# Optimization experiments

Hardware: AMD Instinct MI355X
Metric: run time of the kernel (lower is better)

Reference implementation:

```python
import jax, jax.numpy as jnp
import numpy as np

N_NODES, N_FEAT, HIDDEN, N_EDGES, N_GRAPHS = 50000, 128, 64, 800000, 64
BN_EPS = 1e-5


def setup_inputs() -> dict:
    key = jax.random.key(0)
    ks = jax.random.split(key, 12)
    x = jax.random.normal(ks[0], (N_NODES, N_FEAT), jnp.float32)
    edge_index = jax.random.randint(ks[1], (2, N_EDGES), 0, N_NODES, jnp.int32)
    batch = jnp.sort(jax.random.randint(ks[2], (N_NODES,), 0, N_GRAPHS, jnp.int32))
    s_in = 1.0 / np.sqrt(N_FEAT)
    s_h = 1.0 / np.sqrt(HIDDEN)
    return {
        "x": x,
        "edge_index": edge_index,
        "batch": batch,
        "W_in": jax.random.normal(ks[3], (HIDDEN, N_FEAT), jnp.float32) * s_in,
        "W1": jax.random.normal(ks[4], (HIDDEN, N_FEAT), jnp.float32) * s_in,
        "b1": jnp.zeros((HIDDEN,), jnp.float32),
        "Ws": jax.random.normal(ks[5], (4, HIDDEN, HIDDEN), jnp.float32) * s_h,
        "bs": jnp.zeros((4, HIDDEN), jnp.float32),
        "bn_gamma": jnp.ones((5, HIDDEN), jnp.float32),
        "bn_beta": jnp.zeros((5, HIDDEN), jnp.float32),
        "bn_mean": jnp.zeros((5, HIDDEN), jnp.float32),
        "bn_var": jnp.ones((5, HIDDEN), jnp.float32),
        "lin_w": jax.random.normal(ks[6], (1, HIDDEN), jnp.float32) * s_h,
        "lin_b": jnp.zeros((1,), jnp.float32),
    }


def reference(x, edge_index, batch, W_in, W1, b1, Ws, bs, bn_gamma, bn_beta, bn_mean, bn_var, lin_w, lin_b):
    N = x.shape[0]
    # add self loops (GCNConv default), symmetric normalization D^-1/2 (A+I) D^-1/2
    loop = jnp.arange(N, dtype=edge_index.dtype)
    src = jnp.concatenate([edge_index[0], loop])  # [E+N]
    dst = jnp.concatenate([edge_index[1], loop])
    deg = jax.ops.segment_sum(jnp.ones_like(dst, jnp.float32), dst, num_segments=N)
    dinv = jax.lax.rsqrt(deg)  # deg >= 1 due to self-loops
    norm = dinv[src] * dinv[dst]  # [E+N]

    def gcn(h, W, b):
        h = h @ W.T                          # [N, H]
        msg = h[src] * norm[:, None]          # gather + edge scaling
        out = jax.ops.segment_sum(msg, dst, num_segments=N)  # scatter-add
        return out + b

    def bn(h, i):
        # eval-mode BatchNorm1d with running stats
        return (h - bn_mean[i]) * (bn_gamma[i] * jax.lax.rsqrt(bn_var[i] + BN_EPS)) + bn_beta[i]

    identity = x @ W_in.T  # input projection for residual
    # layer 1 (dropout = identity in eval)
    h = jax.nn.relu(bn(gcn(x, W1, b1), 0)) + identity
    # layers 2-4 with residual
    for i in range(3):
        h = jax.nn.relu(bn(gcn(h, Ws[i], bs[i]), i + 1)) + h
    # layer 5, no residual afterwards
    h = jax.nn.relu(bn(gcn(h, Ws[3], bs[3]), 4))

    # global mean pool over graphs
    sums = jax.ops.segment_sum(h, batch, num_segments=N_GRAPHS)
    cnts = jax.ops.segment_sum(jnp.ones((N,), jnp.float32), batch, num_segments=N_GRAPHS)
    pooled = sums / jnp.maximum(cnts, 1.0)[:, None]  # [G, H]
    return pooled @ lin_w.T + lin_b  # [G, 1]
```

## Files before the change

### kernel.cpp

```cpp
#include <hip/hip_runtime.h>
#include <hip/hip_fp16.h>

#define N_NODES 50000
#define N_FEAT  128
#define HID     64
#define N_EDGES 800000
#define N_GRAPHS 64
#define MAXDEG  64
#define BN_EPS  1e-5f
#define NB256(n) (((n) + 255) / 256)

__global__ __launch_bounds__(256) void k_zero(int* fill) {
    int i = blockIdx.x * 256 + threadIdx.x;
    if (i < N_NODES) fill[i] = 0;
}

#define GE_NB 2500
__global__ __launch_bounds__(256) void k_gemmedge(const int* __restrict__ ei,
                                                  int* fill, unsigned short* __restrict__ colp,
                                                  const float* __restrict__ x,
                                                  const float* __restrict__ W_in,
                                                  const float* __restrict__ W1,
                                                  float* __restrict__ h,
                                                  __half* __restrict__ g16) {
    __shared__ float4 Wt[2][8 * 65];
    __shared__ float4 xs[20 * 32];
    const int bid = blockIdx.x;
    const int t = threadIdx.x;

    const int ebase = bid * 320;
    int s1 = ei[ebase + t];
    int d1 = ei[N_EDGES + ebase + t];
    int k1 = atomicAdd(&fill[d1], 1);
    int s2 = 0, d2 = 0, k2 = MAXDEG;
    if (t < 64) {
        s2 = ei[ebase + 256 + t];
        d2 = ei[N_EDGES + ebase + 256 + t];
        k2 = atomicAdd(&fill[d2], 1);
    }

    const float4* W0v = (const float4*)W_in;
    const float4* W1v = (const float4*)W1;
    const int h2a = t >> 3, k4a = t & 7;
    const int h2b = h2a + 32;
    float4 w0a = W0v[h2a * 32 + k4a];
    float4 w1a = W1v[h2a * 32 + k4a];
    float4 w0b = W0v[h2b * 32 + k4a];
    float4 w1b = W1v[h2b * 32 + k4a];

    const int base = bid * 20;
    const float4* xv = (const float4*)(x + (long long)base * N_FEAT);
    for (int i = t; i < 20 * 32; i += 256) xs[i] = xv[i];

    const int hh = t & 63;
    const int ng = t >> 6;
    float4 a0[5], a1[5];
#pragma unroll
    for (int j = 0; j < 5; ++j) {
        a0[j] = make_float4(0.f, 0.f, 0.f, 0.f);
        a1[j] = make_float4(0.f, 0.f, 0.f, 0.f);
    }

    for (int c = 0; c < 32; c += 8) {
        __syncthreads();
        Wt[0][k4a * 65 + h2a] = w0a;  Wt[1][k4a * 65 + h2a] = w1a;
        Wt[0][k4a * 65 + h2b] = w0b;  Wt[1][k4a * 65 + h2b] = w1b;
        if (c + 8 < 32) {
            w0a = W0v[h2a * 32 + c + 8 + k4a]; w1a = W1v[h2a * 32 + c + 8 + k4a];
            w0b = W0v[h2b * 32 + c + 8 + k4a]; w1b = W1v[h2b * 32 + c + 8 + k4a];
        }
        __syncthreads();
#pragma unroll
        for (int k4 = 0; k4 < 8; ++k4) {
            float4 w0 = Wt[0][k4 * 65 + hh];
            float4 w1 = Wt[1][k4 * 65 + hh];
#pragma unroll
            for (int j = 0; j < 5; ++j) {
                float4 xx = xs[(ng + 4 * j) * 32 + c + k4];
                a0[j].x += w0.x * xx.x; a0[j].y += w0.y * xx.y;
                a0[j].z += w0.z * xx.z; a0[j].w += w0.w * xx.w;
                a1[j].x += w1.x * xx.x; a1[j].y += w1.y * xx.y;
                a1[j].z += w1.z * xx.z; a1[j].w += w1.w * xx.w;
            }
        }
    }
#pragma unroll
    for (int j = 0; j < 5; ++j) {
        int node = base + ng + 4 * j;
        h[node * HID + hh]   = a0[j].x + a0[j].y + a0[j].z + a0[j].w;
        g16[node * HID + hh] = __float2half(a1[j].x + a1[j].y + a1[j].z + a1[j].w);
    }

    if (k1 < MAXDEG) colp[d1 * MAXDEG + k1] = (unsigned short)s1;
    if (k2 < MAXDEG) colp[d2 * MAXDEG + k2] = (unsigned short)s2;
}

__device__ __forceinline__ void acc8s(const uint4 r, float* a, float s) {
    float2 f0 = __half22float2(*(const __half2*)&r.x);
    float2 f1 = __half22float2(*(const __half2*)&r.y);
    float2 f2 = __half22float2(*(const __half2*)&r.z);
    float2 f3 = __half22float2(*(const __half2*)&r.w);
    a[0] += s * f0.x; a[1] += s * f0.y; a[2] += s * f1.x; a[3] += s * f1.y;
    a[4] += s * f2.x; a[5] += s * f2.y; a[6] += s * f3.x; a[7] += s * f3.y;
}

template <bool NSCALE, bool DOGEMM>
__global__ __launch_bounds__(256, 4) void k_gather_fused(const __half* __restrict__ gin,
                                                      const unsigned short* __restrict__ colp,
                                                      const int* __restrict__ fill,
                                                      const float* __restrict__ b,
                                                      const float* __restrict__ gamma,
                                                      const float* __restrict__ beta,
                                                      const float* __restrict__ mean,
                                                      const float* __restrict__ var,
                                                      const float4* __restrict__ res4,
                                                      float4* __restrict__ h4,
                                                      const float* __restrict__ W,
                                                      __half* __restrict__ gout) {
    __shared__ float4 Wt[DOGEMM ? 16 * 65 : 1];
    __shared__ float4 hrow[DOGEMM ? 32 * 17 : 1];

    const int t = threadIdx.x;
    const int wv = t >> 6;
    const int lane = t & 63;
    const int hh8 = lane & 7;
    const int sub = lane >> 3;
    const int nl = wv * 8 + sub;
    const int n = blockIdx.x * 32 + nl;
    const bool nvalid = (n < N_NODES);

    if (DOGEMM) {
        const float4* Wv = (const float4*)W;
        for (int i = t; i < HID * 16; i += 256) {
            int h2 = i >> 4, k4 = i & 15;
            Wt[k4 * 65 + h2] = Wv[i];
        }
        __syncthreads();
    }

    const uint4* gv = (const uint4*)gin;
    const int fl = nvalid ? fill[n] : 0;
    const int deg = fl < MAXDEG ? fl : MAXDEG;

    float a[8];
#pragma unroll
    for (int i = 0; i < 8; ++i) a[i] = 0.f;

    const uint4* cp8 = (const uint4*)(colp + (size_t)n * MAXDEG);

#pragma unroll 1
    for (int rb = 0; rb < MAXDEG; rb += 8) {
        if (!__any(rb < deg)) break;
        if (rb < deg) {
            uint4 cc = cp8[rb >> 3];
            unsigned cw[4] = {cc.x, cc.y, cc.z, cc.w};
            int c[8]; float s[8]; uint4 v[8];
#pragma unroll
            for (int k = 0; k < 8; ++k) {
                bool pk = (rb + k) < deg;
                int col = (int)((cw[k >> 1] >> (16 * (k & 1))) & 0xFFFFu);
                c[k] = pk ? col : 0;
                if (NSCALE) s[k] = pk ? rsqrtf((float)fill[c[k]] + 1.0f) : 0.0f;
                else        s[k] = pk ? 1.0f : 0.0f;
            }
#pragma unroll
            for (int k = 0; k < 8; ++k) v[k] = gv[(size_t)c[k] * 8 + hh8];
#pragma unroll
            for (int k = 0; k < 8; ++k) acc8s(v[k], a, s[k]);
        }
    }

    const float di = rsqrtf((float)fl + 1.0f);
    if (nvalid) acc8s(gv[(size_t)n * 8 + hh8], a, NSCALE ? di : 1.0f);

    float o[8];
    {
        float4 b0 = ((const float4*)b)[hh8 * 2],     b1 = ((const float4*)b)[hh8 * 2 + 1];
        float4 g0 = ((const float4*)gamma)[hh8 * 2], g1 = ((const float4*)gamma)[hh8 * 2 + 1];
        float4 e0 = ((const float4*)beta)[hh8 * 2],  e1 = ((const float4*)beta)[hh8 * 2 + 1];
        float4 m0 = ((const float4*)mean)[hh8 * 2],  m1 = ((const float4*)mean)[hh8 * 2 + 1];
        float4 v0 = ((const float4*)var)[hh8 * 2],   v1 = ((const float4*)var)[hh8 * 2 + 1];
        float bb[8] = {b0.x, b0.y, b0.z, b0.w, b1.x, b1.y, b1.z, b1.w};
        float gg[8] = {g0.x, g0.y, g0.z, g0.w, g1.x, g1.y, g1.z, g1.w};
        float ee[8] = {e0.x, e0.y, e0.z, e0.w, e1.x, e1.y, e1.z, e1.w};
        float mm[8] = {m0.x, m0.y, m0.z, m0.w, m1.x, m1.y, m1.z, m1.w};
        float vv[8] = {v0.x, v0.y, v0.z, v0.w, v1.x, v1.y, v1.z, v1.w};
#pragma unroll
        for (int i = 0; i < 8; ++i) {
            float sc = gg[i] * rsqrtf(vv[i] + BN_EPS);
            float sh = (bb[i] - mm[i]) * sc + ee[i];
            o[i] = fmaxf(fmaf(a[i] * di, sc, sh), 0.f);
        }
    }

    if (res4 != nullptr && nvalid) {
        float4 r0 = res4[(size_t)n * 16 + hh8 * 2];
        float4 r1 = res4[(size_t)n * 16 + hh8 * 2 + 1];
        o[0] += r0.x; o[1] += r0.y; o[2] += r0.z; o[3] += r0.w;
        o[4] += r1.x; o[5] += r1.y; o[6] += r1.z; o[7] += r1.w;
    }

    float4 lo = make_float4(o[0], o[1], o[2], o[3]);
    float4 hi = make_float4(o[4], o[5], o[6], o[7]);
    if (nvalid) {
        h4[(size_t)n * 16 + hh8 * 2]     = lo;
        h4[(size_t)n * 16 + hh8 * 2 + 1] = hi;
    }

    if (DOGEMM) {
        hrow[nl * 17 + hh8 * 2]     = lo;
        hrow[nl * 17 + hh8 * 2 + 1] = hi;
        const int hh = lane;
        const int nb = blockIdx.x * 32 + wv * 8;
        float acc[8];
#pragma unroll
        for (int s8 = 0; s8 < 8; ++s8) acc[s8] = 0.f;
#pragma unroll 2
        for (int k4 = 0; k4 < 16; ++k4) {
            float4 w = Wt[k4 * 65 + hh];
#pragma unroll
            for (int s8 = 0; s8 < 8; ++s8) {
                float4 hv = hrow[(wv * 8 + s8) * 17 + k4];
                acc[s8] += hv.x * w.x + hv.y * w.y + hv.z * w.z + hv.w * w.w;
            }
        }
#pragma unroll
        for (int s8 = 0; s8 < 8; ++s8) {
            int ns = nb + s8;
            if (ns < N_NODES) {
                float dd = rsqrtf((float)fill[ns] + 1.0f);
                gout[(size_t)ns * HID + hh] = __float2half(acc[s8] * dd);
            }
        }
    }
}

__device__ __forceinline__ int lowerb(const int* __restrict__ b, int val) {
    int lo = 0, hi = N_NODES;
    while (lo < hi) {
        int mid = (lo + hi) >> 1;
        if (b[mid] < val) lo = mid + 1; else hi = mid;
    }
    return lo;
}

__global__ __launch_bounds__(1024) void k_poolfinal(const float* __restrict__ h,
                                                    const int* __restrict__ batch,
                                                    const float* __restrict__ lin_w,
                                                    const float* __restrict__ lin_b,
                                                    float* __restrict__ out) {
    __shared__ float red[16][HID];
    int g = blockIdx.x;
    int w = threadIdx.x >> 6;
    int hh = threadIdx.x & 63;
    int start = lowerb(batch, g);
    int end = lowerb(batch, g + 1);
    int len = end - start;
    float acc = 0.f;
    for (int n = start + w; n < end; n += 16) acc += h[n * HID + hh];
    red[w][hh] = acc;
    __syncthreads();
    if (w == 0) {
        float s = 0.f;
#pragma unroll
        for (int i = 0; i < 16; ++i) s += red[i][hh];
        float c = fmaxf((float)len, 1.0f);
        float v = (s / c) * lin_w[hh];
#pragma unroll
        for (int off = 32; off > 0; off >>= 1) v += __shfl_down(v, off);
        if (hh == 0) out[g] = v + lin_b[0];
    }
}

extern "C" void kernel_launch(void* const* d_in, const int* in_sizes, int n_in,
                              void* d_out, int out_size, void* d_ws, size_t ws_size,
                              hipStream_t stream) {
    const float* x     = (const float*)d_in[0];
    const int*   ei    = (const int*)d_in[1];
    const int*   batch = (const int*)d_in[2];
    const float* W_in  = (const float*)d_in[3];
    const float* W1    = (const float*)d_in[4];
    const float* b1    = (const float*)d_in[5];
    const float* Ws    = (const float*)d_in[6];
    const float* bs_   = (const float*)d_in[7];
    const float* bn_g  = (const float*)d_in[8];
    const float* bn_b  = (const float*)d_in[9];
    const float* bn_m  = (const float*)d_in[10];
    const float* bn_v  = (const float*)d_in[11];
    const float* lin_w = (const float*)d_in[12];
    const float* lin_b = (const float*)d_in[13];
    float* out = (float*)d_out;

    char* q = (char*)d_ws;
    int*            fill = (int*)q;             q += (size_t)50048 * 4;
    unsigned short* colp = (unsigned short*)q;  q += (size_t)N_NODES * MAXDEG * 2;
    __half*         g16a = (__half*)q;          q += (size_t)N_NODES * HID * 2;
    __half*         g16b = (__half*)q;          q += (size_t)N_NODES * HID * 2;
    float*          h    = (float*)q;           q += (size_t)N_NODES * HID * 4;

    const int NB_N  = NB256(N_NODES);
    const int NB_GA = (N_NODES + 31) / 32;
    float4* h4 = (float4*)h;

    k_zero<<<NB_N, 256, 0, stream>>>(fill);
    k_gemmedge<<<GE_NB, 256, 0, stream>>>(ei, fill, colp, x, W_in, W1, h, g16a);

    k_gather_fused<true, true><<<NB_GA, 256, 0, stream>>>(
        g16a, colp, fill, b1, bn_g, bn_b, bn_m, bn_v,
        (const float4*)h, h4, Ws + 0 * HID * HID, g16b);

    k_gather_fused<false, true><<<NB_GA, 256, 0, stream>>>(
        g16b, colp, fill, bs_ + 0 * HID,
        bn_g + 1 * HID, bn_b + 1 * HID, bn_m + 1 * HID, bn_v + 1 * HID,
        (const float4*)h, h4, Ws + 1 * HID * HID, g16a);

    k_gather_fused<false, true><<<NB_GA, 256, 0, stream>>>(
        g16a, colp, fill, bs_ + 1 * HID,
        bn_g + 2 * HID, bn_b + 2 * HID, bn_m + 2 * HID, bn_v + 2 * HID,
        (const float4*)h, h4, Ws + 2 * HID * HID, g16b);

    k_gather_fused<false, true><<<NB_GA, 256, 0, stream>>>(
        g16b, colp, fill, bs_ + 2 * HID,
        bn_g + 3 * HID, bn_b + 3 * HID, bn_m + 3 * HID, bn_v + 3 * HID,
        (const float4*)h, h4, Ws + 3 * HID * HID, g16a);

    k_gather_fused<false, false><<<NB_GA, 256, 0, stream>>>(
        g16a, colp, fill, bs_ + 3 * HID,
        bn_g + 4 * HID, bn_b + 4 * HID, bn_m + 4 * HID, bn_v + 4 * HID,
        nullptr, h4, nullptr, nullptr);

    k_poolfinal<<<N_GRAPHS, 1024, 0, stream>>>(h, batch, lin_w, lin_b, out);
}
```

Baseline: 311.0 us.

## Assign one wavefront per node with edge-parallel gather and shuffle reduction

Restructures the fused gather kernel so that each 64-lane wavefront handles one node rather than eight. The eight lane groups each process a different edge and are combined with xor-shuffle reductions. The column indices are loaded once per wave and distributed by shuffle, and the next edge's fetch is software-pipelined ahead of the accumulation. The aim is to balance load across nodes of varying degree and raise memory-level parallelism. The cost is 8x more blocks and a full W transpose into shared memory for every 4 nodes, which adds LDS traffic and per-block overhead. Bounds checks are removed, which relies on N_NODES being divisible by 4.

```diff
diff --git a/kernel.cpp b/kernel.cpp
--- a/kernel.cpp
+++ b/kernel.cpp
@@ -105,7 +105,7 @@
 }
 
 template <bool NSCALE, bool DOGEMM>
-__global__ __launch_bounds__(256, 4) void k_gather_fused(const __half* __restrict__ gin,
+__global__ __launch_bounds__(256) void k_gather_fused(const __half* __restrict__ gin,
                                                       const unsigned short* __restrict__ colp,
                                                       const int* __restrict__ fill,
                                                       const float* __restrict__ b,
@@ -118,16 +118,14 @@
                                                       const float* __restrict__ W,
                                                       __half* __restrict__ gout) {
     __shared__ float4 Wt[DOGEMM ? 16 * 65 : 1];
-    __shared__ float4 hrow[DOGEMM ? 32 * 17 : 1];
+    __shared__ float4 hrow[DOGEMM ? 4 * 17 : 1];
 
     const int t = threadIdx.x;
     const int wv = t >> 6;
     const int lane = t & 63;
+    const int egrp = lane >> 3;
     const int hh8 = lane & 7;
-    const int sub = lane >> 3;
-    const int nl = wv * 8 + sub;
-    const int n = blockIdx.x * 32 + nl;
-    const bool nvalid = (n < N_NODES);
+    const int n = blockIdx.x * 4 + wv;
 
     if (DOGEMM) {
         const float4* Wv = (const float4*)W;
@@ -135,43 +133,52 @@
             int h2 = i >> 4, k4 = i & 15;
             Wt[k4 * 65 + h2] = Wv[i];
         }
-        __syncthreads();
     }
 
     const uint4* gv = (const uint4*)gin;
-    const int fl = nvalid ? fill[n] : 0;
+    const int fl = fill[n];
     const int deg = fl < MAXDEG ? fl : MAXDEG;
 
+    int colall = (int)colp[(size_t)n * MAXDEG + lane];
+    const uint4 vself = gv[(size_t)n * 8 + hh8];
+
     float a[8];
 #pragma unroll
     for (int i = 0; i < 8; ++i) a[i] = 0.f;
 
-    const uint4* cp8 = (const uint4*)(colp + (size_t)n * MAXDEG);
-
+    const int nit = (deg + 7) >> 3;
+
+#define FETCH_E(IT, C, S, V)                                              \
+    {                                                                     \
+        int j = ((IT) << 3) + egrp;                                       \
+        int cc = __shfl(colall, j & 63);                                  \
+        bool pv = j < deg;                                                \
+        C = pv ? cc : 0;                                                  \
+        if (NSCALE) S = pv ? rsqrtf((float)fill[C] + 1.0f) : 0.0f;        \
+        else        S = pv ? 1.0f : 0.0f;                                 \
+        V = gv[(size_t)C * 8 + hh8];                                      \
+    }
+
+    int cA; float sA; uint4 vA;
+    FETCH_E(0, cA, sA, vA);
 #pragma unroll 1
-    for (int rb = 0; rb < MAXDEG; rb += 8) {
-        if (!__any(rb < deg)) break;
-        if (rb < deg) {
-            uint4 cc = cp8[rb >> 3];
-            unsigned cw[4] = {cc.x, cc.y, cc.z, cc.w};
-            int c[8]; float s[8]; uint4 v[8];
-#pragma unroll
-            for (int k = 0; k < 8; ++k) {
-                bool pk = (rb + k) < deg;
-                int col = (int)((cw[k >> 1] >> (16 * (k & 1))) & 0xFFFFu);
-                c[k] = pk ? col : 0;
-                if (NSCALE) s[k] = pk ? rsqrtf((float)fill[c[k]] + 1.0f) : 0.0f;
-                else        s[k] = pk ? 1.0f : 0.0f;
-            }
-#pragma unroll
-            for (int k = 0; k < 8; ++k) v[k] = gv[(size_t)c[k] * 8 + hh8];
-#pragma unroll
-            for (int k = 0; k < 8; ++k) acc8s(v[k], a, s[k]);
-        }
+    for (int it = 0; it + 1 < nit; ++it) {
+        int cB; float sB; uint4 vB;
+        FETCH_E(it + 1, cB, sB, vB);
+        acc8s(vA, a, sA);
+        cA = cB; sA = sB; vA = vB;
+    }
+    if (nit > 0) acc8s(vA, a, sA);
+#undef FETCH_E
+
+#pragma unroll
+    for (int m = 8; m <= 32; m <<= 1) {
+#pragma unroll
+        for (int i = 0; i < 8; ++i) a[i] += __shfl_xor(a[i], m);
     }
 
     const float di = rsqrtf((float)fl + 1.0f);
-    if (nvalid) acc8s(gv[(size_t)n * 8 + hh8], a, NSCALE ? di : 1.0f);
+    acc8s(vself, a, NSCALE ? di : 1.0f);
 
     float o[8];
     {
@@ -193,7 +200,7 @@
         }
     }
 
-    if (res4 != nullptr && nvalid) {
+    if (res4 != nullptr) {
         float4 r0 = res4[(size_t)n * 16 + hh8 * 2];
         float4 r1 = res4[(size_t)n * 16 + hh8 * 2 + 1];
         o[0] += r0.x; o[1] += r0.y; o[2] += r0.z; o[3] += r0.w;
@@ -202,36 +209,25 @@
 
     float4 lo = make_float4(o[0], o[1], o[2], o[3]);
     float4 hi = make_float4(o[4], o[5], o[6], o[7]);
-    if (nvalid) {
+    if (egrp == 0) {
         h4[(size_t)n * 16 + hh8 * 2]     = lo;
         h4[(size_t)n * 16 + hh8 * 2 + 1] = hi;
     }
 
     if (DOGEMM) {
-        hrow[nl * 17 + hh8 * 2]     = lo;
-        hrow[nl * 17 + hh8 * 2 + 1] = hi;
-        const int hh = lane;
-        const int nb = blockIdx.x * 32 + wv * 8;
-        float acc[8];
-#pragma unroll
-        for (int s8 = 0; s8 < 8; ++s8) acc[s8] = 0.f;
+        if (egrp == 0) {
+            hrow[wv * 17 + hh8 * 2]     = lo;
+            hrow[wv * 17 + hh8 * 2 + 1] = hi;
+        }
+        __syncthreads();
+        float acc = 0.f;
 #pragma unroll 2
         for (int k4 = 0; k4 < 16; ++k4) {
-            float4 w = Wt[k4 * 65 + hh];
-#pragma unroll
-            for (int s8 = 0; s8 < 8; ++s8) {
-                float4 hv = hrow[(wv * 8 + s8) * 17 + k4];
-                acc[s8] += hv.x * w.x + hv.y * w.y + hv.z * w.z + hv.w * w.w;
-            }
-        }
-#pragma unroll
-        for (int s8 = 0; s8 < 8; ++s8) {
-            int ns = nb + s8;
-            if (ns < N_NODES) {
-                float dd = rsqrtf((float)fill[ns] + 1.0f);
-                gout[(size_t)ns * HID + hh] = __float2half(acc[s8] * dd);
-            }
-        }
+            float4 w = Wt[k4 * 65 + lane];
+            float4 hv = hrow[wv * 17 + k4];
+            acc += hv.x * w.x + hv.y * w.y + hv.z * w.z + hv.w * w.w;
+        }
+        gout[(size_t)n * HID + lane] = __float2half(acc * di);
     }
 }
 
@@ -299,7 +295,7 @@
     float*          h    = (float*)q;           q += (size_t)N_NODES * HID * 4;
 
     const int NB_N  = NB256(N_NODES);
-    const int NB_GA = (N_NODES + 31) / 32;
+    const int NB_GA = N_NODES / 4;
     float4* h4 = (float4*)h;
 
     k_zero<<<NB_N, 256, 0, stream>>>(fill);
```

After: 374.4 us. 1.2x slower.
